# Performance work log

Hardware: AMD Instinct MI355X
Metric: run time of the kernel (lower is better)

The kernel has to match this reference:

```python
import jax, jax.numpy as jnp
import numpy as np

B, T, C = 2, 2048, 2048
N_HEAD = 16
N_KV_HEAD = 16
HEAD_DIM = C // N_HEAD  # 128
KV_LORA = C // 2        # 1024
KV_PE = KV_LORA // 4    # 256
KV_CONTENT = KV_LORA - KV_PE  # 768
EPS = 1.1920929e-07  # torch.finfo(float32).eps, F.rms_norm default


def _rms_norm(x):
    # unlearned RMSNorm over last dim
    return x * jax.lax.rsqrt(jnp.mean(x * x, axis=-1, keepdims=True) + EPS)


def _apply_rotary(x, cos, sin):
    # x: (B,T,H,D); cos,sin: (1,T,1,D/2)
    d = x.shape[-1] // 2
    x1, x2 = x[..., :d], x[..., d:]
    return jnp.concatenate([x1 * cos + x2 * sin, -x1 * sin + x2 * cos], axis=-1)


def setup_inputs() -> dict:
    key = jax.random.key(0)
    ks = jax.random.split(key, 9)
    x = jax.random.normal(ks[0], (B, T, C), dtype=jnp.float32)
    # realistic RoPE tables (values bounded like real cos/sin)
    half = HEAD_DIM // 2
    inv_freq = 1.0 / (10000.0 ** (np.arange(0, half, dtype=np.float32) / half))
    tpos = np.arange(T, dtype=np.float32)
    ang = np.einsum('t,d->td', tpos, inv_freq)
    cos = jnp.asarray(np.cos(ang))[None, :, None, :]
    sin = jnp.asarray(np.sin(ang))[None, :, None, :]
    s = 0.02
    wq_a = jax.random.normal(ks[1], (C, KV_LORA), dtype=jnp.float32) * s
    wq_b = jax.random.normal(ks[2], (KV_LORA, N_HEAD * HEAD_DIM), dtype=jnp.float32) * s
    wkv_a = jax.random.normal(ks[3], (C, KV_LORA), dtype=jnp.float32) * s
    wk_b = jax.random.normal(ks[4], (KV_CONTENT, N_KV_HEAD * HEAD_DIM), dtype=jnp.float32) * s
    wkpe_b = jax.random.normal(ks[5], (KV_PE, N_KV_HEAD * HEAD_DIM), dtype=jnp.float32) * s
    wv_b = jax.random.normal(ks[6], (KV_CONTENT, N_KV_HEAD * HEAD_DIM), dtype=jnp.float32) * s
    wo = jax.random.normal(ks[7], (C, C), dtype=jnp.float32) * s
    return dict(x=x, cos=cos, sin=sin, wq_a=wq_a, wq_b=wq_b, wkv_a=wkv_a,
                wk_b=wk_b, wkpe_b=wkpe_b, wv_b=wv_b, wo=wo)


def reference(x, cos, sin, wq_a, wq_b, wkv_a, wk_b, wkpe_b, wv_b, wo):
    Bx, Tx, Cx = x.shape
    # low-rank Q path
    q = (x @ wq_a) @ wq_b                      # (B,T,H*D)
    q = q.reshape(Bx, Tx, N_HEAD, HEAD_DIM)
    # low-rank KV path with pe/content split
    kv_latent = x @ wkv_a                       # (B,T,KV_LORA)
    kv_pe = kv_latent[..., :KV_PE]
    kv_content = kv_latent[..., KV_PE:]
    k_content = (kv_content @ wk_b).reshape(Bx, Tx, N_KV_HEAD, HEAD_DIM)
    k_pe = (kv_pe @ wkpe_b).reshape(Bx, Tx, N_KV_HEAD, HEAD_DIM)
    k = k_content + _apply_rotary(k_pe, cos, sin)
    v = (kv_content @ wv_b).reshape(Bx, Tx, N_KV_HEAD, HEAD_DIM)
    # QK RMSNorm (unlearned)
    q = _rms_norm(q)
    k = _rms_norm(k)
    # SDPA, causal (kv_cache=None path); n_head == n_kv_head
    qh = q.transpose(0, 2, 1, 3)  # (B,H,T,D)
    kh = k.transpose(0, 2, 1, 3)
    vh = v.transpose(0, 2, 1, 3)
    scale = 1.0 / jnp.sqrt(jnp.asarray(HEAD_DIM, dtype=x.dtype))
    scores = jnp.einsum('bhqd,bhkd->bhqk', qh, kh) * scale
    causal = jnp.tril(jnp.ones((Tx, Tx), dtype=bool))
    scores = jnp.where(causal[None, None], scores, jnp.asarray(-jnp.inf, dtype=scores.dtype))
    probs = jax.nn.softmax(scores, axis=-1)
    y = jnp.einsum('bhqk,bhkd->bhqd', probs, vh)
    y = y.transpose(0, 2, 1, 3).reshape(Bx, Tx, Cx)
    return y @ wo
```

## Files before the change

### kernel.cpp

```cpp
#include <hip/hip_runtime.h>
#include <cstddef>
#include <cstdint>

#define TT 2048
#define HH 16
#define EPSV 1.1920929e-07f
#define QSCALE 0.08838834764831845f
#define LOG2E 1.4426950408889634f
#define THRL 11.0f

typedef short bfv8 __attribute__((ext_vector_type(8)));
typedef float f32x4 __attribute__((ext_vector_type(4)));

__device__ __forceinline__ short f2bf(float f) {
    unsigned u = __builtin_bit_cast(unsigned, f);
    u += 0x7FFFu + ((u >> 16) & 1u);
    return (short)(u >> 16);
}
__device__ __forceinline__ float bf2f(short s) {
    unsigned u = ((unsigned)(unsigned short)s) << 16;
    return __builtin_bit_cast(float, u);
}
__device__ __forceinline__ bfv8 pack8(const float4 a, const float4 b) {
    bfv8 r;
    r[0]=f2bf(a.x); r[1]=f2bf(a.y); r[2]=f2bf(a.z); r[3]=f2bf(a.w);
    r[4]=f2bf(b.x); r[5]=f2bf(b.y); r[6]=f2bf(b.z); r[7]=f2bf(b.w);
    return r;
}
__device__ __forceinline__ void gload16(const void* g, void* l) {
    __builtin_amdgcn_global_load_lds(
        (const __attribute__((address_space(1))) unsigned int*)g,
        (__attribute__((address_space(3))) unsigned int*)l, 16, 0, 0);
}

__global__ __launch_bounds__(256) void convx(const float* __restrict__ src,
                                             short* __restrict__ dst, int n8)
{
    int i = blockIdx.x * blockDim.x + threadIdx.x;
    int stride = gridDim.x * blockDim.x;
    for (; i < n8; i += stride) {
        float4 a = ((const float4*)src)[2*i], b = ((const float4*)src)[2*i+1];
        ((bfv8*)dst)[i] = pack8(a, b);
    }
}

__global__ __launch_bounds__(256) void wtrans(const float* __restrict__ src,
                                              short* __restrict__ dst, int R, int C)
{
    __shared__ short tile[64][72];
    const int tid = threadIdx.x;
    const int r0 = blockIdx.y * 64, c0 = blockIdx.x * 64;
    {
        const int i = tid >> 2, c = (tid & 3) * 16;
        const float* sp = src + ((size_t)(r0 + i)) * C + c0 + c;
        float4 v0 = ((const float4*)sp)[0], v1 = ((const float4*)sp)[1];
        float4 v2 = ((const float4*)sp)[2], v3 = ((const float4*)sp)[3];
        *(bfv8*)&tile[i][c]     = pack8(v0, v1);
        *(bfv8*)&tile[i][c + 8] = pack8(v2, v3);
    }
    __syncthreads();
    {
        const int j = tid >> 2, rc = (tid & 3) * 16;
        bfv8 g0, g1;
#pragma unroll
        for (int jj = 0; jj < 8; ++jj) { g0[jj] = tile[rc + jj][j]; g1[jj] = tile[rc + 8 + jj][j]; }
        short* dp = dst + ((size_t)(c0 + j)) * R + r0 + rc;
        *(bfv8*)dp       = g0;
        *(bfv8*)(dp + 8) = g1;
    }
}

template<int OUT_MODE>
__global__ __launch_bounds__(256) void gemm_bf16(
    const short* __restrict__ A, int lda,
    const short* __restrict__ B, int ldb,
    void* __restrict__ Cptr, int ldc, int K)
{
    __shared__ short As[2][128 * 32];
    __shared__ short Bs[2][128 * 32];
    const int tid = threadIdx.x;
    const int w = tid >> 6, lane = tid & 63;
    const int lr = lane & 15, lg = lane >> 4;
    const int wr = w >> 1, wc = w & 1;
    const size_t bm = (size_t)blockIdx.y * 128, bn = (size_t)blockIdx.x * 128;

    f32x4 acc[4][4] = {};

    const int r0 = tid >> 2, ch = (tid & 3) * 8;
    const short* aB0 = A + (bm + r0) * (size_t)lda + ch;
    const short* aB1 = aB0 + 64 * (size_t)lda;
    const short* bB0 = B + (bn + r0) * (size_t)ldb + ch;
    const short* bB1 = bB0 + 64 * (size_t)ldb;
    const int wof = w * 512;

    gload16(aB0, As[0] + wof);
    gload16(aB1, As[0] + wof + 2048);
    gload16(bB0, Bs[0] + wof);
    gload16(bB1, Bs[0] + wof + 2048);
    __syncthreads();

    int cur = 0;
    for (int k0 = 0; k0 < K; k0 += 32) {
        if (k0 + 32 < K) {
            gload16(aB0 + k0 + 32, As[cur ^ 1] + wof);
            gload16(aB1 + k0 + 32, As[cur ^ 1] + wof + 2048);
            gload16(bB0 + k0 + 32, Bs[cur ^ 1] + wof);
            gload16(bB1 + k0 + 32, Bs[cur ^ 1] + wof + 2048);
        }
        bfv8 af[4], bfr[4];
#pragma unroll
        for (int i = 0; i < 4; ++i) {
            af[i]  = *(const bfv8*)&As[cur][(wr * 64 + i * 16 + lr) * 32 + lg * 8];
            bfr[i] = *(const bfv8*)&Bs[cur][(wc * 64 + i * 16 + lr) * 32 + lg * 8];
        }
#pragma unroll
        for (int i = 0; i < 4; ++i)
#pragma unroll
            for (int j = 0; j < 4; ++j)
                acc[i][j] = __builtin_amdgcn_mfma_f32_16x16x32_bf16(af[i], bfr[j], acc[i][j], 0, 0, 0);
        __syncthreads();
        cur ^= 1;
    }

    const size_t crow = bm + wr * 64 + 4 * lg;
    const size_t ccol = bn + wc * 64 + lr;
#pragma unroll
    for (int i = 0; i < 4; ++i)
#pragma unroll
        for (int j = 0; j < 4; ++j)
#pragma unroll
            for (int r = 0; r < 4; ++r) {
                size_t off = (crow + i * 16 + r) * (size_t)ldc + ccol + j * 16;
                if (OUT_MODE == 0) ((float*)Cptr)[off] = acc[i][j][r];
                else               ((short*)Cptr)[off] = f2bf(acc[i][j][r]);
            }
}

__global__ __launch_bounds__(256) void finalize_k(
    const short* __restrict__ kc, const short* __restrict__ pe,
    const float* __restrict__ cosb, const float* __restrict__ sinb,
    short* __restrict__ kb)
{
    const int gw = blockIdx.x * 4 + (threadIdx.x >> 6);
    const int l = threadIdx.x & 63;
    const int r = gw >> 4, h = gw & 15;
    const int t = r & (TT - 1), b = r >> 11;
    const size_t kcb = (size_t)r * 4096 + h * 128;
    const size_t peb = (size_t)r * 2048 + h * 128;

    float x1 = bf2f(pe[peb + l]), x2 = bf2f(pe[peb + 64 + l]);
    float c = cosb[t * 64 + l], s = sinb[t * 64 + l];
    float lo = bf2f(kc[kcb + l])      + x1 * c + x2 * s;
    float hi = bf2f(kc[kcb + 64 + l]) - x1 * s + x2 * c;

    float ss = lo * lo + hi * hi;
#pragma unroll
    for (int o = 32; o; o >>= 1) ss += __shfl_xor(ss, o);
    float rr = rsqrtf(ss * (1.0f / 128.0f) + EPSV);
    const size_t ob = (((size_t)b * HH + h) * TT + t) * 128;
    kb[ob + l]      = f2bf(lo * rr);
    kb[ob + 64 + l] = f2bf(hi * rr);
}

__global__ __launch_bounds__(256) void finalize_q(
    const short* __restrict__ qi, short* __restrict__ qo)
{
    const int gw = blockIdx.x * 4 + (threadIdx.x >> 6);
    const int l = threadIdx.x & 63;
    const int r = gw >> 4, h = gw & 15;
    const int t = r & (TT - 1), b = r >> 11;
    const short* qp = qi + (size_t)r * 2048 + h * 128 + 2 * l;
    float a = bf2f(qp[0]), bq = bf2f(qp[1]);
    float ss = a * a + bq * bq;
#pragma unroll
    for (int o = 32; o; o >>= 1) ss += __shfl_xor(ss, o);
    float rr = rsqrtf(ss * (1.0f / 128.0f) + EPSV) * (QSCALE * LOG2E);
    short* op = qo + (((size_t)b * HH + h) * TT + t) * 128 + 2 * l;
    op[0] = f2bf(a * rr);
    op[1] = f2bf(bq * rr);
}

__global__ __launch_bounds__(256) void vtrans(
    const short* __restrict__ src, short* __restrict__ dst)
{
    __shared__ short tile[64][72];
    const int tt = blockIdx.x, dt = blockIdx.y, bh = blockIdx.z;
    const int tid = threadIdx.x;
    {
        const int i = tid >> 2, c = (tid & 3) * 16;
        const size_t sb = ((size_t)((bh >> 4) * TT + tt * 64 + i)) * 4096 + 2048 + (bh & 15) * 128 + dt * 64 + c;
        *(bfv8*)&tile[i][c]     = *(const bfv8*)&src[sb];
        *(bfv8*)&tile[i][c + 8] = *(const bfv8*)&src[sb + 8];
    }
    __syncthreads();
    {
        const int j = tid >> 2, rc = (tid & 3) * 16;
        bfv8 g0, g1;
#pragma unroll
        for (int jj = 0; jj < 8; ++jj) { g0[jj] = tile[rc + jj][j]; g1[jj] = tile[rc + 8 + jj][j]; }
        const size_t db = (((size_t)bh) * 128 + dt * 64 + j) * TT + tt * 64 + rc;
        *(bfv8*)&dst[db]     = g0;
        *(bfv8*)&dst[db + 8] = g1;
    }
}

__device__ __forceinline__ void qk_tile(const short* __restrict__ Ks,
    const bfv8 aq[4], f32x4 s[4], int lr, int lg)
{
#pragma unroll
    for (int ct = 0; ct < 4; ++ct) {
        f32x4 a = {0.f, 0.f, 0.f, 0.f};
        const int row = ct * 16 + lr;
#pragma unroll
        for (int ks = 0; ks < 4; ++ks) {
            const bfv8 bk = *(const bfv8*)&Ks[row * 128 + (((ks * 4 + lg) ^ (row & 7)) * 8)];
            a = __builtin_amdgcn_mfma_f32_16x16x32_bf16(aq[ks], bk, a, 0, 0, 0);
        }
        s[ct] = a;
    }
}

__device__ __forceinline__ void mask_diag(f32x4 s[4], int lr, int lg, int w)
{
    const int rq = w * 16 + 4 * lg;
#pragma unroll
    for (int ct = 0; ct < 4; ++ct)
#pragma unroll
        for (int r = 0; r < 4; ++r)
            if (ct * 16 + lr > rq + r) s[ct][r] = -__builtin_inff();
}

__device__ __forceinline__ void softmax1(f32x4 s[4], float m[4], float l[4], f32x4 o[8])
{
    float mt[4];
#pragma unroll
    for (int r = 0; r < 4; ++r) mt[r] = fmaxf(fmaxf(s[0][r], s[1][r]), fmaxf(s[2][r], s[3][r]));
#pragma unroll
    for (int off = 1; off < 16; off <<= 1)
#pragma unroll
        for (int r = 0; r < 4; ++r) mt[r] = fmaxf(mt[r], __shfl_xor(mt[r], off));
    float g = fmaxf(fmaxf(mt[0] - m[0], mt[1] - m[1]), fmaxf(mt[2] - m[2], mt[3] - m[3]));
    if (!__all(g <= THRL)) {
        float alpha[4];
#pragma unroll
        for (int r = 0; r < 4; ++r) {
            float mn = fmaxf(m[r], mt[r]);
            alpha[r] = exp2f(m[r] - mn);
            m[r] = mn; l[r] *= alpha[r];
        }
#pragma unroll
        for (int dt = 0; dt < 8; ++dt) {
            o[dt][0] *= alpha[0]; o[dt][1] *= alpha[1];
            o[dt][2] *= alpha[2]; o[dt][3] *= alpha[3];
        }
    }
#pragma unroll
    for (int ct = 0; ct < 4; ++ct)
#pragma unroll
        for (int r = 0; r < 4; ++r) s[ct][r] = exp2f(s[ct][r] - m[r]);
    float rs[4];
#pragma unroll
    for (int r = 0; r < 4; ++r) rs[r] = (s[0][r] + s[1][r]) + (s[2][r] + s[3][r]);
#pragma unroll
    for (int off = 1; off < 16; off <<= 1)
#pragma unroll
        for (int r = 0; r < 4; ++r) rs[r] += __shfl_xor(rs[r], off);
#pragma unroll
    for (int r = 0; r < 4; ++r) l[r] += rs[r];
}

__device__ __forceinline__ void softmax2(
    f32x4 s1[4], f32x4 s2[4],
    float m1[4], float l1[4], float m2[4], float l2[4],
    f32x4 o1[8], f32x4 o2[8])
{
    float mt1[4], mt2[4];
#pragma unroll
    for (int r = 0; r < 4; ++r) {
        mt1[r] = fmaxf(fmaxf(s1[0][r], s1[1][r]), fmaxf(s1[2][r], s1[3][r]));
        mt2[r] = fmaxf(fmaxf(s2[0][r], s2[1][r]), fmaxf(s2[2][r], s2[3][r]));
    }
#pragma unroll
    for (int off = 1; off < 16; off <<= 1)
#pragma unroll
        for (int r = 0; r < 4; ++r) {
            mt1[r] = fmaxf(mt1[r], __shfl_xor(mt1[r], off));
            mt2[r] = fmaxf(mt2[r], __shfl_xor(mt2[r], off));
        }
    float g1 = fmaxf(fmaxf(mt1[0] - m1[0], mt1[1] - m1[1]), fmaxf(mt1[2] - m1[2], mt1[3] - m1[3]));
    float g2 = fmaxf(fmaxf(mt2[0] - m2[0], mt2[1] - m2[1]), fmaxf(mt2[2] - m2[2], mt2[3] - m2[3]));
    if (!__all(g1 <= THRL)) {
        float alpha[4];
#pragma unroll
        for (int r = 0; r < 4; ++r) {
            float mn = fmaxf(m1[r], mt1[r]);
            alpha[r] = exp2f(m1[r] - mn);
            m1[r] = mn; l1[r] *= alpha[r];
        }
#pragma unroll
        for (int dt = 0; dt < 8; ++dt) {
            o1[dt][0] *= alpha[0]; o1[dt][1] *= alpha[1];
            o1[dt][2] *= alpha[2]; o1[dt][3] *= alpha[3];
        }
    }
    if (!__all(g2 <= THRL)) {
        float alpha[4];
#pragma unroll
        for (int r = 0; r < 4; ++r) {
            float mn = fmaxf(m2[r], mt2[r]);
            alpha[r] = exp2f(m2[r] - mn);
            m2[r] = mn; l2[r] *= alpha[r];
        }
#pragma unroll
        for (int dt = 0; dt < 8; ++dt) {
            o2[dt][0] *= alpha[0]; o2[dt][1] *= alpha[1];
            o2[dt][2] *= alpha[2]; o2[dt][3] *= alpha[3];
        }
    }
#pragma unroll
    for (int ct = 0; ct < 4; ++ct)
#pragma unroll
        for (int r = 0; r < 4; ++r) {
            s1[ct][r] = exp2f(s1[ct][r] - m1[r]);
            s2[ct][r] = exp2f(s2[ct][r] - m2[r]);
        }
    float rs1[4], rs2[4];
#pragma unroll
    for (int r = 0; r < 4; ++r) {
        rs1[r] = (s1[0][r] + s1[1][r]) + (s1[2][r] + s1[3][r]);
        rs2[r] = (s2[0][r] + s2[1][r]) + (s2[2][r] + s2[3][r]);
    }
#pragma unroll
    for (int off = 1; off < 16; off <<= 1)
#pragma unroll
        for (int r = 0; r < 4; ++r) {
            rs1[r] += __shfl_xor(rs1[r], off);
            rs2[r] += __shfl_xor(rs2[r], off);
        }
#pragma unroll
    for (int r = 0; r < 4; ++r) { l1[r] += rs1[r]; l2[r] += rs2[r]; }
}

__device__ __forceinline__ void pv_tile(const short* __restrict__ Vs,
    short (&Psw)[16][72], const f32x4 s[4], f32x4 o[8], int lr, int lg)
{
#pragma unroll
    for (int ct = 0; ct < 4; ++ct)
#pragma unroll
        for (int r = 0; r < 4; ++r)
            Psw[4 * lg + r][ct * 16 + lr] = f2bf(s[ct][r]);
    const bfv8 pa0 = *(const bfv8*)&Psw[lr][lg * 8];
    const bfv8 pa1 = *(const bfv8*)&Psw[lr][32 + lg * 8];
#pragma unroll
    for (int dt = 0; dt < 8; ++dt) {
        const int row = dt * 16 + lr;
        const bfv8 bv0 = *(const bfv8*)&Vs[row * 64 + ((lg ^ (row & 7)) * 8)];
        const bfv8 bv1 = *(const bfv8*)&Vs[row * 64 + (((4 + lg) ^ (row & 7)) * 8)];
        o[dt] = __builtin_amdgcn_mfma_f32_16x16x32_bf16(pa0, bv0, o[dt], 0, 0, 0);
        o[dt] = __builtin_amdgcn_mfma_f32_16x16x32_bf16(pa1, bv1, o[dt], 0, 0, 0);
    }
}

__global__ __launch_bounds__(256) void attn_kernel(
    const short* __restrict__ qg, const short* __restrict__ kg,
    const short* __restrict__ vg, short* __restrict__ y)
{
    __shared__ short Ks[2][64 * 128];
    __shared__ short Vs[2][128 * 64];
    __shared__ short Ps[4][16][72];

    const int lin = blockIdx.x + 16 * blockIdx.y + 256 * blockIdx.z;
    const int work = (lin & 7) * 64 + (lin >> 3);
    const int pi = work & 15, h = (work >> 4) & 15, b = work >> 8;
    const int qt1 = pi, qt2 = 31 - pi;
    const int tid = threadIdx.x, w = tid >> 6, lane = tid & 63;
    const int lr = lane & 15, lg = lane >> 4;

    const size_t tok0 = ((size_t)b * HH + h) * TT;
    bfv8 aq1[4], aq2[4];
    {
        const size_t q1 = (tok0 + qt1 * 64 + w * 16 + lr) * 128;
        const size_t q2 = (tok0 + qt2 * 64 + w * 16 + lr) * 128;
#pragma unroll
        for (int ks = 0; ks < 4; ++ks) {
            aq1[ks] = *(const bfv8*)&qg[q1 + ks * 32 + lg * 8];
            aq2[ks] = *(const bfv8*)&qg[q2 + ks * 32 + lg * 8];
        }
    }
    f32x4 o1[8] = {}; f32x4 o2[8] = {};
    float m1[4], l1[4], m2[4], l2[4];
#pragma unroll
    for (int r = 0; r < 4; ++r) { m1[r] = m2[r] = -__builtin_inff(); l1[r] = l2[r] = 0.f; }

    const size_t vhead = ((size_t)b * HH + h) * (size_t)128 * TT;
    const int krow = tid >> 4, kub = tid & 15;
    const int vrow = tid >> 3, vub = tid & 7;
    const int wof = w * 512;

#define STAGE_KV(KT, BUF)                                                          \
    {                                                                              \
        const size_t kbase = (tok0 + (KT) * 64) * 128;                             \
        _Pragma("unroll")                                                          \
        for (int p = 0; p < 4; ++p) {                                              \
            int row = p * 16 + krow;                                               \
            int u = kub ^ (row & 7);                                               \
            gload16(kg + kbase + row * 128 + u * 8, Ks[BUF] + wof + p * 2048);     \
            int rv = p * 32 + vrow;                                                \
            int uv = vub ^ (rv & 7);                                               \
            gload16(vg + vhead + (size_t)rv * TT + (KT) * 64 + uv * 8,             \
                    Vs[BUF] + wof + p * 2048);                                     \
        }                                                                          \
    }

    STAGE_KV(0, 0);
    __syncthreads();

    int cur = 0;
    for (int kt = 0; kt <= qt1; ++kt) {
        if (kt < qt2) STAGE_KV(kt + 1, cur ^ 1);
        f32x4 s1[4], s2[4];
        qk_tile(Ks[cur], aq2, s2, lr, lg);
        qk_tile(Ks[cur], aq1, s1, lr, lg);
        if (kt == qt1) mask_diag(s1, lr, lg, w);
        softmax2(s1, s2, m1, l1, m2, l2, o1, o2);
        pv_tile(Vs[cur], Ps[w], s2, o2, lr, lg);
        pv_tile(Vs[cur], Ps[w], s1, o1, lr, lg);
        __syncthreads();
        cur ^= 1;
    }
    for (int kt = qt1 + 1; kt <= qt2; ++kt) {
        if (kt < qt2) STAGE_KV(kt + 1, cur ^ 1);
        f32x4 s2[4];
        qk_tile(Ks[cur], aq2, s2, lr, lg);
        if (kt == qt2) mask_diag(s2, lr, lg, w);
        softmax1(s2, m2, l2, o2);
        pv_tile(Vs[cur], Ps[w], s2, o2, lr, lg);
        __syncthreads();
        cur ^= 1;
    }

#pragma unroll
    for (int r = 0; r < 4; ++r) {
        float inv1 = 1.0f / l1[r], inv2 = 1.0f / l2[r];
        const size_t y1 = ((size_t)b * TT + qt1 * 64 + w * 16 + 4 * lg + r) * 2048 + h * 128 + lr;
        const size_t y2 = ((size_t)b * TT + qt2 * 64 + w * 16 + 4 * lg + r) * 2048 + h * 128 + lr;
#pragma unroll
        for (int dt = 0; dt < 8; ++dt) {
            y[y1 + dt * 16] = f2bf(o1[dt][r] * inv1);
            y[y2 + dt * 16] = f2bf(o2[dt][r] * inv2);
        }
    }
}

extern "C" void kernel_launch(void* const* d_in, const int* in_sizes, int n_in,
                              void* d_out, int out_size, void* d_ws, size_t ws_size,
                              hipStream_t stream)
{
    const float* x      = (const float*)d_in[0];
    const float* cosb   = (const float*)d_in[1];
    const float* sinb   = (const float*)d_in[2];
    const float* wq_a   = (const float*)d_in[3];
    const float* wq_b   = (const float*)d_in[4];
    const float* wkv_a  = (const float*)d_in[5];
    const float* wk_b   = (const float*)d_in[6];
    const float* wkpe_b = (const float*)d_in[7];
    const float* wv_b   = (const float*)d_in[8];
    const float* wo     = (const float*)d_in[9];

    short* wsp = (short*)d_ws;
    short* W1  = wsp;
    short* W2  = wsp + 4194304;
    short* W3  = wsp + 7340032;
    short* W4  = wsp + 7864320;
    short* W5  = wsp + 9961472;
    short* C1  = wsp + 14155776;
    short* KV2 = wsp + 22544384;
    short* KPE = wsp + 39321600;
    short* KB  = wsp + 47710208;
    short* VB  = wsp + 56098816;
    short* XB  = (short*)d_out;

    dim3 blk(256);

    convx<<<2048, blk, 0, stream>>>(x, XB, 1048576);
    wtrans<<<dim3(16, 32), blk, 0, stream>>>(wq_a,   W1,                2048, 1024);
    wtrans<<<dim3(16, 32), blk, 0, stream>>>(wkv_a,  W1 + 1024 * 2048,  2048, 1024);
    wtrans<<<dim3(32, 12), blk, 0, stream>>>(wk_b,   W2,                 768, 2048);
    wtrans<<<dim3(32, 12), blk, 0, stream>>>(wv_b,   W2 + 2048 * 768,    768, 2048);
    wtrans<<<dim3(32,  4), blk, 0, stream>>>(wkpe_b, W3,                 256, 2048);
    wtrans<<<dim3(32, 16), blk, 0, stream>>>(wq_b,   W4,                1024, 2048);
    wtrans<<<dim3(32, 32), blk, 0, stream>>>(wo,     W5,                2048, 2048);

    gemm_bf16<1><<<dim3(16, 32), blk, 0, stream>>>(XB, 2048, W1, 2048, C1, 2048, 2048);
    gemm_bf16<1><<<dim3(32, 32), blk, 0, stream>>>(C1 + 1280, 2048, W2, 768, KV2, 4096, 768);
    gemm_bf16<1><<<dim3(16, 32), blk, 0, stream>>>(C1 + 1024, 2048, W3, 256, KPE, 2048, 256);

    finalize_k<<<16384, blk, 0, stream>>>(KV2, KPE, cosb, sinb, KB);
    vtrans<<<dim3(32, 2, 32), blk, 0, stream>>>(KV2, VB);

    gemm_bf16<1><<<dim3(16, 32), blk, 0, stream>>>(C1, 2048, W4, 1024, KPE, 2048, 1024);
    finalize_q<<<16384, blk, 0, stream>>>(KPE, KV2);

    attn_kernel<<<dim3(16, 16, 2), blk, 0, stream>>>(KV2, KB, VB, C1);

    gemm_bf16<0><<<dim3(16, 32), blk, 0, stream>>>(C1, 2048, W5, 2048, d_out, 2048, 2048);
}
```

Measured before the change: 357.1 us.

## Fuse Q RMSNorm into attention, single-buffer KV, use hardware exp2 and swizzle reductions

Drops the separate finalize_q kernel. The attention kernel now reads raw Q from the Q-projection output and applies RMSNorm and the scale in registers. The attention inner loop moves from double-buffered async KV staging to a single buffer with a sync after each load, which halves LDS use but removes the overlap of loads with compute. Softmax uses raw v_exp_f32 inline asm and ds_swizzle for the row reductions instead of exp2f and shfl_xor, and P is packed with v_cvt_pk_bf16_f32. Swizzle index math is simplified by hoisting lr&7.

```diff
diff --git a/kernel.cpp b/kernel.cpp
--- a/kernel.cpp
+++ b/kernel.cpp
@@ -32,6 +32,23 @@
         (const __attribute__((address_space(1))) unsigned int*)g,
         (__attribute__((address_space(3))) unsigned int*)l, 16, 0, 0);
 }
+__device__ __forceinline__ unsigned cvtpk(float a, float b) {
+    unsigned r;
+    asm("v_cvt_pk_bf16_f32 %0, %1, %2" : "=v"(r) : "v"(a), "v"(b));
+    return r;
+}
+__device__ __forceinline__ float fexp2(float x) {
+    float y;
+    asm volatile("v_exp_f32 %0, %1\n\ts_nop 1" : "=v"(y) : "v"(x));
+    return y;
+}
+#define SWZF(V, IMM) __builtin_bit_cast(float, __builtin_amdgcn_ds_swizzle(__builtin_bit_cast(int, (V)), IMM))
+#define RMAX_RND(M, IMM) { M[0]=fmaxf(M[0],SWZF(M[0],IMM)); M[1]=fmaxf(M[1],SWZF(M[1],IMM)); \
+                           M[2]=fmaxf(M[2],SWZF(M[2],IMM)); M[3]=fmaxf(M[3],SWZF(M[3],IMM)); }
+#define RMAX4(M) RMAX_RND(M,0x041F) RMAX_RND(M,0x081F) RMAX_RND(M,0x101F) RMAX_RND(M,0x201F)
+#define RSUM_RND(M, IMM) { M[0]+=SWZF(M[0],IMM); M[1]+=SWZF(M[1],IMM); \
+                           M[2]+=SWZF(M[2],IMM); M[3]+=SWZF(M[3],IMM); }
+#define RSUM4(M) RSUM_RND(M,0x041F) RSUM_RND(M,0x081F) RSUM_RND(M,0x101F) RSUM_RND(M,0x201F)
 
 __global__ __launch_bounds__(256) void convx(const float* __restrict__ src,
                                              short* __restrict__ dst, int n8)
@@ -162,24 +179,6 @@
     kb[ob + 64 + l] = f2bf(hi * rr);
 }
 
-__global__ __launch_bounds__(256) void finalize_q(
-    const short* __restrict__ qi, short* __restrict__ qo)
-{
-    const int gw = blockIdx.x * 4 + (threadIdx.x >> 6);
-    const int l = threadIdx.x & 63;
-    const int r = gw >> 4, h = gw & 15;
-    const int t = r & (TT - 1), b = r >> 11;
-    const short* qp = qi + (size_t)r * 2048 + h * 128 + 2 * l;
-    float a = bf2f(qp[0]), bq = bf2f(qp[1]);
-    float ss = a * a + bq * bq;
-#pragma unroll
-    for (int o = 32; o; o >>= 1) ss += __shfl_xor(ss, o);
-    float rr = rsqrtf(ss * (1.0f / 128.0f) + EPSV) * (QSCALE * LOG2E);
-    short* op = qo + (((size_t)b * HH + h) * TT + t) * 128 + 2 * l;
-    op[0] = f2bf(a * rr);
-    op[1] = f2bf(bq * rr);
-}
-
 __global__ __launch_bounds__(256) void vtrans(
     const short* __restrict__ src, short* __restrict__ dst)
 {
@@ -207,13 +206,14 @@
 __device__ __forceinline__ void qk_tile(const short* __restrict__ Ks,
     const bfv8 aq[4], f32x4 s[4], int lr, int lg)
 {
+    const int swz = lr & 7;
 #pragma unroll
     for (int ct = 0; ct < 4; ++ct) {
         f32x4 a = {0.f, 0.f, 0.f, 0.f};
         const int row = ct * 16 + lr;
 #pragma unroll
         for (int ks = 0; ks < 4; ++ks) {
-            const bfv8 bk = *(const bfv8*)&Ks[row * 128 + (((ks * 4 + lg) ^ (row & 7)) * 8)];
+            const bfv8 bk = *(const bfv8*)&Ks[row * 128 + (((ks * 4 + lg) ^ swz) * 8)];
             a = __builtin_amdgcn_mfma_f32_16x16x32_bf16(aq[ks], bk, a, 0, 0, 0);
         }
         s[ct] = a;
@@ -235,17 +235,14 @@
     float mt[4];
 #pragma unroll
     for (int r = 0; r < 4; ++r) mt[r] = fmaxf(fmaxf(s[0][r], s[1][r]), fmaxf(s[2][r], s[3][r]));
-#pragma unroll
-    for (int off = 1; off < 16; off <<= 1)
-#pragma unroll
-        for (int r = 0; r < 4; ++r) mt[r] = fmaxf(mt[r], __shfl_xor(mt[r], off));
+    RMAX4(mt)
     float g = fmaxf(fmaxf(mt[0] - m[0], mt[1] - m[1]), fmaxf(mt[2] - m[2], mt[3] - m[3]));
     if (!__all(g <= THRL)) {
         float alpha[4];
 #pragma unroll
         for (int r = 0; r < 4; ++r) {
             float mn = fmaxf(m[r], mt[r]);
-            alpha[r] = exp2f(m[r] - mn);
+            alpha[r] = fexp2(m[r] - mn);
             m[r] = mn; l[r] *= alpha[r];
         }
 #pragma unroll
@@ -257,14 +254,11 @@
 #pragma unroll
     for (int ct = 0; ct < 4; ++ct)
 #pragma unroll
-        for (int r = 0; r < 4; ++r) s[ct][r] = exp2f(s[ct][r] - m[r]);
+        for (int r = 0; r < 4; ++r) s[ct][r] = fexp2(s[ct][r] - m[r]);
     float rs[4];
 #pragma unroll
     for (int r = 0; r < 4; ++r) rs[r] = (s[0][r] + s[1][r]) + (s[2][r] + s[3][r]);
-#pragma unroll
-    for (int off = 1; off < 16; off <<= 1)
-#pragma unroll
-        for (int r = 0; r < 4; ++r) rs[r] += __shfl_xor(rs[r], off);
+    RSUM4(rs)
 #pragma unroll
     for (int r = 0; r < 4; ++r) l[r] += rs[r];
 }
@@ -280,13 +274,7 @@
         mt1[r] = fmaxf(fmaxf(s1[0][r], s1[1][r]), fmaxf(s1[2][r], s1[3][r]));
         mt2[r] = fmaxf(fmaxf(s2[0][r], s2[1][r]), fmaxf(s2[2][r], s2[3][r]));
     }
-#pragma unroll
-    for (int off = 1; off < 16; off <<= 1)
-#pragma unroll
-        for (int r = 0; r < 4; ++r) {
-            mt1[r] = fmaxf(mt1[r], __shfl_xor(mt1[r], off));
-            mt2[r] = fmaxf(mt2[r], __shfl_xor(mt2[r], off));
-        }
+    RMAX4(mt1) RMAX4(mt2)
     float g1 = fmaxf(fmaxf(mt1[0] - m1[0], mt1[1] - m1[1]), fmaxf(mt1[2] - m1[2], mt1[3] - m1[3]));
     float g2 = fmaxf(fmaxf(mt2[0] - m2[0], mt2[1] - m2[1]), fmaxf(mt2[2] - m2[2], mt2[3] - m2[3]));
     if (!__all(g1 <= THRL)) {
@@ -294,7 +282,7 @@
 #pragma unroll
         for (int r = 0; r < 4; ++r) {
             float mn = fmaxf(m1[r], mt1[r]);
-            alpha[r] = exp2f(m1[r] - mn);
+            alpha[r] = fexp2(m1[r] - mn);
             m1[r] = mn; l1[r] *= alpha[r];
         }
 #pragma unroll
@@ -308,7 +296,7 @@
 #pragma unroll
         for (int r = 0; r < 4; ++r) {
             float mn = fmaxf(m2[r], mt2[r]);
-            alpha[r] = exp2f(m2[r] - mn);
+            alpha[r] = fexp2(m2[r] - mn);
             m2[r] = mn; l2[r] *= alpha[r];
         }
 #pragma unroll
@@ -321,8 +309,8 @@
     for (int ct = 0; ct < 4; ++ct)
 #pragma unroll
         for (int r = 0; r < 4; ++r) {
-            s1[ct][r] = exp2f(s1[ct][r] - m1[r]);
-            s2[ct][r] = exp2f(s2[ct][r] - m2[r]);
+            s1[ct][r] = fexp2(s1[ct][r] - m1[r]);
+            s2[ct][r] = fexp2(s2[ct][r] - m2[r]);
         }
     float rs1[4], rs2[4];
 #pragma unroll
@@ -330,13 +318,7 @@
         rs1[r] = (s1[0][r] + s1[1][r]) + (s1[2][r] + s1[3][r]);
         rs2[r] = (s2[0][r] + s2[1][r]) + (s2[2][r] + s2[3][r]);
     }
-#pragma unroll
-    for (int off = 1; off < 16; off <<= 1)
-#pragma unroll
-        for (int r = 0; r < 4; ++r) {
-            rs1[r] += __shfl_xor(rs1[r], off);
-            rs2[r] += __shfl_xor(rs2[r], off);
-        }
+    RSUM4(rs1) RSUM4(rs2)
 #pragma unroll
     for (int r = 0; r < 4; ++r) { l1[r] += rs1[r]; l2[r] += rs2[r]; }
 }
@@ -345,17 +327,22 @@
     short (&Psw)[16][72], const f32x4 s[4], f32x4 o[8], int lr, int lg)
 {
 #pragma unroll
-    for (int ct = 0; ct < 4; ++ct)
-#pragma unroll
-        for (int r = 0; r < 4; ++r)
-            Psw[4 * lg + r][ct * 16 + lr] = f2bf(s[ct][r]);
+    for (int ct = 0; ct < 4; ++ct) {
+        unsigned u0 = cvtpk(s[ct][0], s[ct][1]);
+        unsigned u1 = cvtpk(s[ct][2], s[ct][3]);
+        Psw[4 * lg + 0][ct * 16 + lr] = (short)u0;
+        Psw[4 * lg + 1][ct * 16 + lr] = (short)(u0 >> 16);
+        Psw[4 * lg + 2][ct * 16 + lr] = (short)u1;
+        Psw[4 * lg + 3][ct * 16 + lr] = (short)(u1 >> 16);
+    }
     const bfv8 pa0 = *(const bfv8*)&Psw[lr][lg * 8];
     const bfv8 pa1 = *(const bfv8*)&Psw[lr][32 + lg * 8];
+    const int swz = lr & 7;
 #pragma unroll
     for (int dt = 0; dt < 8; ++dt) {
         const int row = dt * 16 + lr;
-        const bfv8 bv0 = *(const bfv8*)&Vs[row * 64 + ((lg ^ (row & 7)) * 8)];
-        const bfv8 bv1 = *(const bfv8*)&Vs[row * 64 + (((4 + lg) ^ (row & 7)) * 8)];
+        const bfv8 bv0 = *(const bfv8*)&Vs[row * 64 + ((lg ^ swz) * 8)];
+        const bfv8 bv1 = *(const bfv8*)&Vs[row * 64 + (((4 + lg) ^ swz) * 8)];
         o[dt] = __builtin_amdgcn_mfma_f32_16x16x32_bf16(pa0, bv0, o[dt], 0, 0, 0);
         o[dt] = __builtin_amdgcn_mfma_f32_16x16x32_bf16(pa1, bv1, o[dt], 0, 0, 0);
     }
@@ -365,8 +352,8 @@
     const short* __restrict__ qg, const short* __restrict__ kg,
     const short* __restrict__ vg, short* __restrict__ y)
 {
-    __shared__ short Ks[2][64 * 128];
-    __shared__ short Vs[2][128 * 64];
+    __shared__ short Ks[64 * 128];
+    __shared__ short Vs[128 * 64];
     __shared__ short Ps[4][16][72];
 
     const int lin = blockIdx.x + 16 * blockIdx.y + 256 * blockIdx.z;
@@ -377,66 +364,76 @@
     const int lr = lane & 15, lg = lane >> 4;
 
     const size_t tok0 = ((size_t)b * HH + h) * TT;
+
     bfv8 aq1[4], aq2[4];
     {
-        const size_t q1 = (tok0 + qt1 * 64 + w * 16 + lr) * 128;
-        const size_t q2 = (tok0 + qt2 * 64 + w * 16 + lr) * 128;
+        const size_t q1 = ((size_t)b * TT + qt1 * 64 + w * 16 + lr) * 2048 + h * 128;
+        const size_t q2 = ((size_t)b * TT + qt2 * 64 + w * 16 + lr) * 2048 + h * 128;
 #pragma unroll
         for (int ks = 0; ks < 4; ++ks) {
             aq1[ks] = *(const bfv8*)&qg[q1 + ks * 32 + lg * 8];
             aq2[ks] = *(const bfv8*)&qg[q2 + ks * 32 + lg * 8];
         }
-    }
+#pragma unroll
+        for (int st = 0; st < 2; ++st) {
+            bfv8* aq = st ? aq2 : aq1;
+            float ss = 0.f;
+#pragma unroll
+            for (int ks = 0; ks < 4; ++ks)
+#pragma unroll
+                for (int j = 0; j < 8; ++j) { float f = bf2f(aq[ks][j]); ss = fmaf(f, f, ss); }
+            ss += __shfl_xor(ss, 16);
+            ss += __shfl_xor(ss, 32);
+            float rr = rsqrtf(ss * (1.0f / 128.0f) + EPSV) * (QSCALE * LOG2E);
+#pragma unroll
+            for (int ks = 0; ks < 4; ++ks)
+#pragma unroll
+                for (int j = 0; j < 4; ++j) {
+                    unsigned u = cvtpk(bf2f(aq[ks][2 * j]) * rr, bf2f(aq[ks][2 * j + 1]) * rr);
+                    aq[ks][2 * j]     = (short)u;
+                    aq[ks][2 * j + 1] = (short)(u >> 16);
+                }
+        }
+    }
+
     f32x4 o1[8] = {}; f32x4 o2[8] = {};
     float m1[4], l1[4], m2[4], l2[4];
 #pragma unroll
     for (int r = 0; r < 4; ++r) { m1[r] = m2[r] = -__builtin_inff(); l1[r] = l2[r] = 0.f; }
 
     const size_t vhead = ((size_t)b * HH + h) * (size_t)128 * TT;
-    const int krow = tid >> 4, kub = tid & 15;
-    const int vrow = tid >> 3, vub = tid & 7;
+    const int krow = tid >> 4, kub = (tid & 15) ^ (krow & 7);
+    const int vrow = tid >> 3, vub = (tid & 7) ^ (vrow & 7);
     const int wof = w * 512;
 
-#define STAGE_KV(KT, BUF)                                                          \
-    {                                                                              \
-        const size_t kbase = (tok0 + (KT) * 64) * 128;                             \
-        _Pragma("unroll")                                                          \
-        for (int p = 0; p < 4; ++p) {                                              \
-            int row = p * 16 + krow;                                               \
-            int u = kub ^ (row & 7);                                               \
-            gload16(kg + kbase + row * 128 + u * 8, Ks[BUF] + wof + p * 2048);     \
-            int rv = p * 32 + vrow;                                                \
-            int uv = vub ^ (rv & 7);                                               \
-            gload16(vg + vhead + (size_t)rv * TT + (KT) * 64 + uv * 8,             \
-                    Vs[BUF] + wof + p * 2048);                                     \
-        }                                                                          \
-    }
-
-    STAGE_KV(0, 0);
-    __syncthreads();
-
-    int cur = 0;
-    for (int kt = 0; kt <= qt1; ++kt) {
-        if (kt < qt2) STAGE_KV(kt + 1, cur ^ 1);
-        f32x4 s1[4], s2[4];
-        qk_tile(Ks[cur], aq2, s2, lr, lg);
-        qk_tile(Ks[cur], aq1, s1, lr, lg);
-        if (kt == qt1) mask_diag(s1, lr, lg, w);
-        softmax2(s1, s2, m1, l1, m2, l2, o1, o2);
-        pv_tile(Vs[cur], Ps[w], s2, o2, lr, lg);
-        pv_tile(Vs[cur], Ps[w], s1, o1, lr, lg);
+    for (int kt = 0; kt <= qt2; ++kt) {
+        {
+            const size_t kbase = (tok0 + kt * 64) * 128;
+#pragma unroll
+            for (int p = 0; p < 4; ++p) {
+                gload16(kg + kbase + (p * 16 + krow) * 128 + kub * 8, Ks + wof + p * 2048);
+                gload16(vg + vhead + (size_t)(p * 32 + vrow) * TT + kt * 64 + vub * 8,
+                        Vs + wof + p * 2048);
+            }
+        }
         __syncthreads();
-        cur ^= 1;
-    }
-    for (int kt = qt1 + 1; kt <= qt2; ++kt) {
-        if (kt < qt2) STAGE_KV(kt + 1, cur ^ 1);
-        f32x4 s2[4];
-        qk_tile(Ks[cur], aq2, s2, lr, lg);
-        if (kt == qt2) mask_diag(s2, lr, lg, w);
-        softmax1(s2, m2, l2, o2);
-        pv_tile(Vs[cur], Ps[w], s2, o2, lr, lg);
+
+        if (kt <= qt1) {
+            f32x4 s1[4], s2[4];
+            qk_tile(Ks, aq2, s2, lr, lg);
+            qk_tile(Ks, aq1, s1, lr, lg);
+            if (kt == qt1) mask_diag(s1, lr, lg, w);
+            softmax2(s1, s2, m1, l1, m2, l2, o1, o2);
+            pv_tile(Vs, Ps[w], s2, o2, lr, lg);
+            pv_tile(Vs, Ps[w], s1, o1, lr, lg);
+        } else {
+            f32x4 s2[4];
+            qk_tile(Ks, aq2, s2, lr, lg);
+            if (kt == qt2) mask_diag(s2, lr, lg, w);
+            softmax1(s2, m2, l2, o2);
+            pv_tile(Vs, Ps[w], s2, o2, lr, lg);
+        }
         __syncthreads();
-        cur ^= 1;
     }
 
 #pragma unroll
@@ -499,9 +496,8 @@
     vtrans<<<dim3(32, 2, 32), blk, 0, stream>>>(KV2, VB);
 
     gemm_bf16<1><<<dim3(16, 32), blk, 0, stream>>>(C1, 2048, W4, 1024, KPE, 2048, 1024);
-    finalize_q<<<16384, blk, 0, stream>>>(KPE, KV2);
-
-    attn_kernel<<<dim3(16, 16, 2), blk, 0, stream>>>(KV2, KB, VB, C1);
+
+    attn_kernel<<<dim3(16, 16, 2), blk, 0, stream>>>(KPE, KB, VB, C1);
 
     gemm_bf16<0><<<dim3(16, 32), blk, 0, stream>>>(C1, 2048, W5, 2048, d_out, 2048, 2048);
 }
```

Result: faster. 348.9 us (-2.3%).
